# Optimization experiments

Measured on AMD Instinct MI355X. Metric: run time of the kernel, lower is better.

Reference implementation:

```python
import math
import jax, jax.numpy as jnp
import numpy as np

B, T, C, H = 4, 2048, 1024, 16
HS = C // H


def setup_inputs() -> dict:
    key = jax.random.key(0)
    ks = jax.random.split(key, 5)
    s_in = 1.0 / math.sqrt(C)
    return {
        "x": jax.random.normal(ks[0], (B, T, C), dtype=jnp.float32),
        "w_attn": jax.random.normal(ks[1], (C, 3 * C), dtype=jnp.float32) * s_in,
        "b_attn": jax.random.normal(ks[2], (3 * C,), dtype=jnp.float32) * 0.02,
        "w_proj": jax.random.normal(ks[3], (C, C), dtype=jnp.float32) * s_in,
        "b_proj": jax.random.normal(ks[4], (C,), dtype=jnp.float32) * 0.02,
    }


def reference(x, w_attn, b_attn, w_proj, b_proj):
    Bx, Tx, Cx = x.shape
    hs = Cx // H
    qkv = x @ w_attn + b_attn  # [B, T, 3C]
    q, k, v = jnp.split(qkv, 3, axis=-1)
    # [B, H, T, hs]
    q = q.reshape(Bx, Tx, H, hs).transpose(0, 2, 1, 3)
    k = k.reshape(Bx, Tx, H, hs).transpose(0, 2, 1, 3)
    v = v.reshape(Bx, Tx, H, hs).transpose(0, 2, 1, 3)
    scale = 1.0 / math.sqrt(hs)
    att = jnp.einsum("bhqd,bhkd->bhqk", q, k) * scale  # [B, H, T, T]
    causal = jnp.tril(jnp.ones((Tx, Tx), dtype=bool))
    att = jnp.where(causal, att, -jnp.inf)
    att = jax.nn.softmax(att, axis=-1)
    y = jnp.einsum("bhqk,bhkd->bhqd", att, v)  # [B, H, T, hs]
    y = y.transpose(0, 2, 1, 3).reshape(Bx, Tx, Cx)
    return y @ w_proj + b_proj
```

## Files before the change

### kernel.cpp

```cpp
#include <hip/hip_runtime.h>
#include <stdint.h>

#define Bn 4
#define Tn 2048
#define Cn 1024
#define Hn 16
#define HSn 64
#define Mn (Bn*Tn)
#define N1n (3*Cn)

typedef unsigned short u16;
typedef unsigned int u32;
typedef __attribute__((ext_vector_type(8))) short short8;
typedef __attribute__((ext_vector_type(4))) float f32x4;
typedef __attribute__((ext_vector_type(16))) float f32x16;

#define QSCf (0.125f * 1.44269504f)

__device__ __forceinline__ u16 f2bf(float f){
  u32 u = __float_as_uint(f);
  u += 0x7fffu + ((u >> 16) & 1u);
  return (u16)(u >> 16);
}

__device__ __forceinline__ u32 pkbf(float lo, float hi_){
  u32 r; asm("v_cvt_pk_bf16_f32 %0, %1, %2" : "=v"(r) : "v"(lo), "v"(hi_)); return r;
}

__device__ __forceinline__ float fexp2(float x){
  float r; asm("v_exp_f32 %0, %1" : "=v"(r) : "v"(x)); return r;
}

__device__ __forceinline__ float fmax3(float a, float b, float c){
  float r; asm("v_max3_f32 %0, %1, %2, %3" : "=v"(r) : "v"(a), "v"(b), "v"(c)); return r;
}

__device__ __forceinline__ void plswap(u32 &a, u32 &b){
  auto r = __builtin_amdgcn_permlane32_swap(a, b, false, false);
  a = r[0]; b = r[1];
}

__device__ __forceinline__ void gload_lds16(const void* g, void* l){
  __builtin_amdgcn_global_load_lds(
      (const __attribute__((address_space(1))) u32*)g,
      (__attribute__((address_space(3))) u32*)l, 16, 0, 0);
}

#define BARRIER() __builtin_amdgcn_s_barrier()
#define CFENCE() asm volatile("" ::: "memory")

__device__ __forceinline__ void tcvt_body(const float* __restrict__ in,
                                          u16* __restrict__ out,
                                          int R, int Cc, int bxx, int byy,
                                          float sh[64][68]){
  int tid = threadIdx.x;
  int c0 = bxx*64, r0 = byy*64;
  int rr = tid >> 4, c4 = (tid & 15) * 4;
  #pragma unroll
  for (int p=0;p<4;p++){
    int r = rr + 16*p;
    *(float4*)&sh[r][c4] = *(const float4*)&in[(size_t)(r0+r)*Cc + c0 + c4];
  }
  __syncthreads();
  #pragma unroll
  for (int p=0;p<4;p++){
    int oc = rr + 16*p;
    u32 w0 = (u32)f2bf(sh[c4+0][oc]) | ((u32)f2bf(sh[c4+1][oc]) << 16);
    u32 w1 = (u32)f2bf(sh[c4+2][oc]) | ((u32)f2bf(sh[c4+3][oc]) << 16);
    uint2 pk; pk.x = w0; pk.y = w1;
    *(uint2*)&out[(size_t)(c0+oc)*R + r0 + c4] = pk;
  }
}

__global__ __launch_bounds__(256)
void k_pre(const float* __restrict__ x, const float* __restrict__ wa,
           const float* __restrict__ wp, u16* __restrict__ xb,
           u16* __restrict__ waT, u16* __restrict__ wpT){
  __shared__ float sh[64][68];
  int bid = blockIdx.x;
  if (bid < 4096){
    int i = bid*256 + threadIdx.x;
    const float4* p = (const float4*)(x) + (size_t)i*2;
    float4 a = p[0], b = p[1];
    uint4 r;
    r.x = (u32)f2bf(a.x) | ((u32)f2bf(a.y) << 16);
    r.y = (u32)f2bf(a.z) | ((u32)f2bf(a.w) << 16);
    r.z = (u32)f2bf(b.x) | ((u32)f2bf(b.y) << 16);
    r.w = (u32)f2bf(b.z) | ((u32)f2bf(b.w) << 16);
    *((uint4*)(xb) + i) = r;
  } else if (bid < 4096 + 768){
    int b2 = bid - 4096;
    tcvt_body(wa, waT, Cn, N1n, b2 % 48, b2 / 48, sh);
  } else {
    int b3 = bid - 4864;
    tcvt_body(wp, wpT, Cn, Cn, b3 % 16, b3 / 16, sh);
  }
}

template <int MODE>
__global__ __launch_bounds__(256, 2)
void k_gemm2(const u16* __restrict__ A, const u16* __restrict__ Bt,
             const float* __restrict__ bias, void* __restrict__ Cout,
             u16* __restrict__ vt, int Nn_, int byPerXcd)
{
  extern __shared__ char smem[];
  const int nkt = 16;
  int tid = threadIdx.x;
  int wave = tid >> 6, lane = tid & 63, g = lane >> 4, cl = lane & 15;
  int wm = wave >> 1, wn = wave & 1;

  int xcd = blockIdx.x & 7, idx = blockIdx.x >> 3;
  int by = xcd * byPerXcd + (idx % byPerXcd);
  int bx = idx / byPerXcd;
  int m0 = by * 128, n0 = bx * 128;

  int srow = tid >> 3;
  int scolb = (tid & 7) << 4;
  int ssw = scolb ^ ((srow & 7) << 4);
  const char* Agp = (const char*)A  + (size_t)(m0 + srow) * 2048 + ssw;
  const char* Bgp = (const char*)Bt + (size_t)(n0 + srow) * 2048 + ssw;

  #define STG(t_, b_) { \
    const char* ag = Agp + (size_t)(t_)*128; \
    const char* bg = Bgp + (size_t)(t_)*128; \
    char* ab = smem + (b_)*32768 + (wave<<10); \
    char* bb = ab + 16384; \
    gload_lds16(ag,          ab); \
    gload_lds16(ag+ 65536,   ab+4096); \
    gload_lds16(ag+131072,   ab+8192); \
    gload_lds16(ag+196608,   ab+12288); \
    gload_lds16(bg,          bb); \
    gload_lds16(bg+ 65536,   bb+4096); \
    gload_lds16(bg+131072,   bb+8192); \
    gload_lds16(bg+196608,   bb+12288); }

  f32x4 acc[4][4];
  #pragma unroll
  for (int i=0;i<4;i++)
    #pragma unroll
    for (int j=0;j<4;j++) acc[i][j] = (f32x4){0.f,0.f,0.f,0.f};

  STG(0, 0);

  for (int t=0; t<nkt; ++t){
    int b = t & 1;
    if (t+1 < nkt){
      STG(t+1, b^1);
      asm volatile("s_waitcnt vmcnt(8)" ::: "memory");
    } else {
      asm volatile("s_waitcnt vmcnt(0)" ::: "memory");
    }
    BARRIER(); CFENCE();
    const char* Asb = smem + b*32768;
    const char* Bsb = Asb + 16384;
    short8 a[4][2], bq[4][2];
    #pragma unroll
    for (int i=0;i<4;i++){
      int row = wm*64 + i*16 + cl;
      #pragma unroll
      for (int ks=0;ks<2;ks++)
        a[i][ks] = *(const short8*)(Asb + row*128 + ((ks*64 + g*16) ^ ((row&7)<<4)));
    }
    #pragma unroll
    for (int j=0;j<4;j++){
      int row = wn*64 + j*16 + cl;
      #pragma unroll
      for (int ks=0;ks<2;ks++)
        bq[j][ks] = *(const short8*)(Bsb + row*128 + ((ks*64 + g*16) ^ ((row&7)<<4)));
    }
    asm volatile("s_waitcnt lgkmcnt(0)" ::: "memory");
    __builtin_amdgcn_s_setprio(1);
    #pragma unroll
    for (int ks=0;ks<2;ks++)
      #pragma unroll
      for (int i=0;i<4;i++)
        #pragma unroll
        for (int j=0;j<4;j++)
          acc[i][j] = __builtin_amdgcn_mfma_f32_16x16x32_bf16(a[i][ks], bq[j][ks], acc[i][j], 0, 0, 0);
    __builtin_amdgcn_s_setprio(0);
    CFENCE(); BARRIER(); CFENCE();
  }
  #undef STG

  #pragma unroll
  for (int jj=0;jj<4;jj++){
    int col = n0 + wn*64 + jj*16 + cl;
    float bj = bias[col];
    if (MODE == 0){
      #pragma unroll
      for (int i=0;i<4;i++){
        int rowb = m0 + wm*64 + i*16 + g*4;
        #pragma unroll
        for (int r=0;r<4;r++)
          ((float*)Cout)[(size_t)(rowb+r)*Nn_ + col] = acc[i][jj][r] + bj;
      }
    } else if (col < 2*Cn){
      float sc = (col < Cn) ? QSCf : 1.0f;
      #pragma unroll
      for (int i=0;i<4;i++){
        int rowb = m0 + wm*64 + i*16 + g*4;
        #pragma unroll
        for (int r=0;r<4;r++)
          ((u16*)Cout)[(size_t)(rowb+r)*Nn_ + col] = f2bf((acc[i][jj][r] + bj) * sc);
      }
    } else {
      int hd = col - 2*Cn;
      #pragma unroll
      for (int i=0;i<4;i++){
        int rowb = m0 + wm*64 + i*16 + g*4;
        int bb = rowb >> 11, tt = rowb & 2047;
        u16* dst = vt + (((size_t)(bb*16 + (hd>>6)))*64 + (hd&63))*2048 + tt;
        uint2 pk;
        pk.x = (u32)f2bf(acc[i][jj][0]+bj) | ((u32)f2bf(acc[i][jj][1]+bj) << 16);
        pk.y = (u32)f2bf(acc[i][jj][2]+bj) | ((u32)f2bf(acc[i][jj][3]+bj) << 16);
        *(uint2*)dst = pk;
      }
    }
  }
}

__global__ __launch_bounds__(256, 4)
void k_attn(const u16* __restrict__ qkv, const u16* __restrict__ vt, u16* __restrict__ yb){
  __shared__ __align__(16) u16 Ks[2][64*64];
  __shared__ __align__(16) u16 Vs[2][64*64];
  int tid = threadIdx.x, wave = tid >> 6, lane = tid & 63;
  int ql = lane & 31, hi = lane >> 5;
  int blk = blockIdx.x;
  int xcd = blk & 7, rest = blk >> 3;
  int bh  = xcd + 8*(rest & 7);
  int qtsel = rest >> 3;
  int a_ = qtsel & 3, g_ = qtsel >> 2;
  int qt = (g_==0) ? (15 - a_) : (g_==1) ? (7 - a_) : (g_==2) ? (8 + a_) : a_;
  int b = bh >> 4, h = bh & 15;

  const u16* Kbase = qkv + (size_t)b*Tn*N1n + Cn + h*HSn;
  const u16* Vbase = vt  + (size_t)bh*HSn*Tn;

  auto STAGE = [&](int bufi, int kt){
    int kb_ = kt*64;
    #pragma unroll
    for (int it=0; it<2; ++it){
      int off = it*4096 + tid*16;
      int row = off >> 7;
      int cb  = off & 127;
      int gc  = (cb ^ ((row & 7) << 4)) >> 1;
      gload_lds16(Kbase + (size_t)(kb_ + row)*N1n + gc,
                  (char*)&Ks[bufi][0] + it*4096 + (wave << 10));
      gload_lds16(Vbase + (size_t)row*Tn + kb_ + gc,
                  (char*)&Vs[bufi][0] + it*4096 + (wave << 10));
    }
  };

  int q0 = qt * 128;
  int qw0 = q0 + wave*32;
  int qg  = qw0 + ql;
  int ntiles = 2*qt + 2;

  const u16* Qp = qkv + (size_t)(b*Tn + qg)*N1n + h*HSn;
  short8 qf[4];
  #pragma unroll
  for (int dc=0; dc<4; ++dc) qf[dc] = *(const short8*)&Qp[dc*16 + hi*8];

  f32x16 accO[2];
  #pragma unroll
  for (int f=0; f<2; ++f)
    #pragma unroll
    for (int r=0; r<16; ++r) accO[f][r] = 0.f;
  float m_ = -1e30f, l_ = 0.f;

  STAGE(0, 0);
  asm volatile("s_waitcnt vmcnt(0)" ::: "memory");
  __syncthreads();
  int buf = 0;

  for (int kt=0; kt<ntiles; ++kt){
    if (kt+1 < ntiles) STAGE(buf^1, kt+1);
    const char* Ksb = (const char*)&Ks[buf][0];
    const char* Vsb = (const char*)&Vs[buf][0];
    #pragma unroll
    for (int ksub=0; ksub<2; ++ksub){
      int kbase = kt*64 + ksub*32;
      if (kbase <= qw0 + 31){
        f32x16 s;
        #pragma unroll
        for (int r=0; r<16; ++r) s[r] = 0.f;
        __builtin_amdgcn_s_setprio(1);
        #pragma unroll
        for (int dc=0; dc<4; ++dc){
          short8 kf = *(const short8*)(Ksb + ((ksub*32 + ql) << 7)
                          + ((dc*32 + hi*16) ^ ((ql & 7) << 4)));
          s = __builtin_amdgcn_mfma_f32_32x32x16_bf16(kf, qf[dc], s, 0, 0, 0);
        }
        __builtin_amdgcn_s_setprio(0);
        float p[16];
        if (kbase + 31 > qw0){
          #pragma unroll
          for (int r=0; r<16; ++r){
            int krow = kbase + (r&3) + 8*(r>>2) + 4*hi;
            p[r] = (krow > qg) ? -1e30f : s[r];
          }
        } else {
          #pragma unroll
          for (int r=0; r<16; ++r) p[r] = s[r];
        }
        float r0 = fmax3(p[0], p[1], p[2]);
        float r1 = fmax3(p[3], p[4], p[5]);
        float r2 = fmax3(p[6], p[7], p[8]);
        float r3 = fmax3(p[9], p[10], p[11]);
        float r4 = fmax3(p[12], p[13], p[14]);
        float tm = fmaxf(fmax3(r0, r1, r2), fmax3(r3, r4, p[15]));
        { u32 ua = __float_as_uint(tm), ub = ua; plswap(ua, ub);
          tm = fmaxf(__uint_as_float(ua), __uint_as_float(ub)); }
        if (!__all(tm - m_ <= 8.0f)){
          float mn = fmaxf(m_, tm);
          float al = fexp2(m_ - mn);
          m_ = mn; l_ *= al;
          #pragma unroll
          for (int f=0; f<2; ++f)
            #pragma unroll
            for (int r=0; r<16; ++r) accO[f][r] *= al;
        }
        float ls = 0.f;
        #pragma unroll
        for (int r=0; r<16; ++r){ float e = fexp2(p[r] - m_); p[r] = e; ls += e; }
        { u32 ua = __float_as_uint(ls), ub = ua; plswap(ua, ub);
          l_ += __uint_as_float(ua) + __uint_as_float(ub); }
        #pragma unroll
        for (int ks=0; ks<2; ++ks){
          int pb = ks*8;
          u32 w0 = pkbf(p[pb+0], p[pb+1]);
          u32 w1 = pkbf(p[pb+2], p[pb+3]);
          u32 w2 = pkbf(p[pb+4], p[pb+5]);
          u32 w3 = pkbf(p[pb+6], p[pb+7]);
          plswap(w0, w2);
          plswap(w1, w3);
          union { u32 w[4]; short8 v; } pu;
          pu.w[0] = w0; pu.w[1] = w1; pu.w[2] = w2; pu.w[3] = w3;
          __builtin_amdgcn_s_setprio(1);
          #pragma unroll
          for (int f=0; f<2; ++f){
            short8 vf = *(const short8*)(Vsb + ((f*32 + ql) << 7)
                            + ((ksub*64 + ks*32 + hi*16) ^ ((ql & 7) << 4)));
            accO[f] = __builtin_amdgcn_mfma_f32_32x32x16_bf16(vf, pu.v, accO[f], 0, 0, 0);
          }
          __builtin_amdgcn_s_setprio(0);
        }
      }
    }
    asm volatile("s_waitcnt vmcnt(0)" ::: "memory");
    __syncthreads();
    buf ^= 1;
  }

  float rl = 1.0f / l_;
  u16* yp = yb + (size_t)(b*Tn + qg)*Cn + h*HSn;
  #pragma unroll
  for (int f=0; f<2; ++f)
    #pragma unroll
    for (int rq=0; rq<4; ++rq){
      int d0 = f*32 + rq*8 + hi*4;
      float v0 = accO[f][rq*4+0]*rl, v1 = accO[f][rq*4+1]*rl;
      float v2 = accO[f][rq*4+2]*rl, v3 = accO[f][rq*4+3]*rl;
      uint2 pk2;
      pk2.x = (u32)f2bf(v0) | ((u32)f2bf(v1) << 16);
      pk2.y = (u32)f2bf(v2) | ((u32)f2bf(v3) << 16);
      *(uint2*)&yp[d0] = pk2;
    }
}

extern "C" void kernel_launch(void* const* d_in, const int* in_sizes, int n_in,
                              void* d_out, int out_size, void* d_ws, size_t ws_size,
                              hipStream_t stream)
{
  const float* x      = (const float*)d_in[0];
  const float* w_attn = (const float*)d_in[1];
  const float* b_attn = (const float*)d_in[2];
  const float* w_proj = (const float*)d_in[3];
  const float* b_proj = (const float*)d_in[4];
  float* out = (float*)d_out;
  char* ws = (char*)d_ws;

  size_t off = 0;
  u16* xb  = (u16*)(ws + off); off += (size_t)Mn*Cn*2;
  u16* waT = (u16*)(ws + off); off += (size_t)N1n*Cn*2;
  u16* wpT = (u16*)(ws + off); off += (size_t)Cn*Cn*2;
  u16* qkv = (u16*)(ws + off); off += (size_t)Mn*N1n*2;
  u16* vt  = (u16*)(ws + off); off += (size_t)Bn*Hn*HSn*Tn*2;
  u16* yb  = (u16*)(ws + off); off += (size_t)Mn*Cn*2;

  (void)hipFuncSetAttribute((const void*)k_gemm2<1>,
        hipFuncAttributeMaxDynamicSharedMemorySize, 65536);
  (void)hipFuncSetAttribute((const void*)k_gemm2<0>,
        hipFuncAttributeMaxDynamicSharedMemorySize, 65536);

  k_pre<<<dim3(5120), 256, 0, stream>>>(x, w_attn, w_proj, xb, waT, wpT);
  k_gemm2<1><<<dim3((Mn/128)*(N1n/128)), 256, 65536, stream>>>(xb, waT, b_attn, qkv, vt, N1n, 8);
  k_attn<<<dim3(1024), 256, 0, stream>>>(qkv, vt, yb);
  k_gemm2<0><<<dim3((Mn/128)*(Cn/128)), 256, 65536, stream>>>(yb, wpT, b_proj, out, nullptr, Cn, 8);
}
```

Measured before the change: 142.4 us.

## Process two 32-row query strips per wave to reuse K/V fragments

The attention kernel now gives each wave 64 query rows, held as two 32-row strips with separate online-softmax state. This doubles the query tile per block to 256 and halves the grid to 512 blocks. K and V fragments are loaded from LDS once and shared by both strips, which cuts LDS traffic and K/V staging per query row. Launch bounds drop to 2 blocks per SM to make room for the doubled registers. Fewer blocks and coarser causal tiles may hurt occupancy and load balance.

New measurement: 159.7 us. 12.1% more time.

```diff
diff --git a/kernel.cpp b/kernel.cpp
--- a/kernel.cpp
+++ b/kernel.cpp
@@ -219,7 +219,7 @@
   }
 }
 
-__global__ __launch_bounds__(256, 4)
+__global__ __launch_bounds__(256, 2)
 void k_attn(const u16* __restrict__ qkv, const u16* __restrict__ vt, u16* __restrict__ yb){
   __shared__ __align__(16) u16 Ks[2][64*64];
   __shared__ __align__(16) u16 Vs[2][64*64];
@@ -228,9 +228,8 @@
   int blk = blockIdx.x;
   int xcd = blk & 7, rest = blk >> 3;
   int bh  = xcd + 8*(rest & 7);
-  int qtsel = rest >> 3;
-  int a_ = qtsel & 3, g_ = qtsel >> 2;
-  int qt = (g_==0) ? (15 - a_) : (g_==1) ? (7 - a_) : (g_==2) ? (8 + a_) : a_;
+  int sel = rest >> 3;
+  int qt  = (sel < 4) ? (7 - sel) : (sel - 4);
   int b = bh >> 4, h = bh & 15;
 
   const u16* Kbase = qkv + (size_t)b*Tn*N1n + Cn + h*HSn;
@@ -251,22 +250,77 @@
     }
   };
 
-  int q0 = qt * 128;
-  int qw0 = q0 + wave*32;
-  int qg  = qw0 + ql;
-  int ntiles = 2*qt + 2;
-
-  const u16* Qp = qkv + (size_t)(b*Tn + qg)*N1n + h*HSn;
-  short8 qf[4];
-  #pragma unroll
-  for (int dc=0; dc<4; ++dc) qf[dc] = *(const short8*)&Qp[dc*16 + hi*8];
-
-  f32x16 accO[2];
-  #pragma unroll
-  for (int f=0; f<2; ++f)
-    #pragma unroll
-    for (int r=0; r<16; ++r) accO[f][r] = 0.f;
-  float m_ = -1e30f, l_ = 0.f;
+  int q0 = qt * 256;
+  int qw0A = q0 + wave*64;
+  int qw0B = qw0A + 32;
+  int qgA = qw0A + ql, qgB = qw0B + ql;
+  int ntiles = 4*qt + 4;
+
+  const u16* QpA = qkv + (size_t)(b*Tn + qgA)*N1n + h*HSn;
+  const u16* QpB = qkv + (size_t)(b*Tn + qgB)*N1n + h*HSn;
+  short8 qfA[4], qfB[4];
+  #pragma unroll
+  for (int dc=0; dc<4; ++dc){
+    qfA[dc] = *(const short8*)&QpA[dc*16 + hi*8];
+    qfB[dc] = *(const short8*)&QpB[dc*16 + hi*8];
+  }
+
+  f32x16 oA0, oA1, oB0, oB1;
+  #pragma unroll
+  for (int r=0; r<16; ++r){ oA0[r]=0.f; oA1[r]=0.f; oB0[r]=0.f; oB1[r]=0.f; }
+  float mA = -1e30f, lA = 0.f, mB = -1e30f, lB = 0.f;
+
+  auto SMPV = [&](f32x16& s, int qg_, int qw0_, float& m_, float& l_,
+                  f32x16& o0, f32x16& o1, int kbase,
+                  short8 vf00, short8 vf01, short8 vf10, short8 vf11){
+    float p[16];
+    if (kbase + 31 > qw0_){
+      #pragma unroll
+      for (int r=0; r<16; ++r){
+        int krow = kbase + (r&3) + 8*(r>>2) + 4*hi;
+        p[r] = (krow > qg_) ? -1e30f : s[r];
+      }
+    } else {
+      #pragma unroll
+      for (int r=0; r<16; ++r) p[r] = s[r];
+    }
+    float r0 = fmax3(p[0], p[1], p[2]);
+    float r1 = fmax3(p[3], p[4], p[5]);
+    float r2 = fmax3(p[6], p[7], p[8]);
+    float r3 = fmax3(p[9], p[10], p[11]);
+    float r4 = fmax3(p[12], p[13], p[14]);
+    float tm = fmaxf(fmax3(r0, r1, r2), fmax3(r3, r4, p[15]));
+    { u32 ua = __float_as_uint(tm), ub = ua; plswap(ua, ub);
+      tm = fmaxf(__uint_as_float(ua), __uint_as_float(ub)); }
+    if (!__all(tm - m_ <= 8.0f)){
+      float mn = fmaxf(m_, tm);
+      float al = fexp2(m_ - mn);
+      m_ = mn; l_ *= al;
+      #pragma unroll
+      for (int r=0; r<16; ++r){ o0[r] *= al; o1[r] *= al; }
+    }
+    float ls = 0.f;
+    #pragma unroll
+    for (int r=0; r<16; ++r){ float e = fexp2(p[r] - m_); p[r] = e; ls += e; }
+    { u32 ua = __float_as_uint(ls), ub = ua; plswap(ua, ub);
+      l_ += __uint_as_float(ua) + __uint_as_float(ub); }
+    #pragma unroll
+    for (int ks=0; ks<2; ++ks){
+      int pb = ks*8;
+      u32 w0 = pkbf(p[pb+0], p[pb+1]);
+      u32 w1 = pkbf(p[pb+2], p[pb+3]);
+      u32 w2 = pkbf(p[pb+4], p[pb+5]);
+      u32 w3 = pkbf(p[pb+6], p[pb+7]);
+      plswap(w0, w2);
+      plswap(w1, w3);
+      union { u32 w[4]; short8 v; } pu;
+      pu.w[0] = w0; pu.w[1] = w1; pu.w[2] = w2; pu.w[3] = w3;
+      __builtin_amdgcn_s_setprio(1);
+      o0 = __builtin_amdgcn_mfma_f32_32x32x16_bf16(ks ? vf10 : vf00, pu.v, o0, 0, 0, 0);
+      o1 = __builtin_amdgcn_mfma_f32_32x32x16_bf16(ks ? vf11 : vf01, pu.v, o1, 0, 0, 0);
+      __builtin_amdgcn_s_setprio(0);
+    }
+  };
 
   STAGE(0, 0);
   asm volatile("s_waitcnt vmcnt(0)" ::: "memory");
@@ -280,71 +334,35 @@
     #pragma unroll
     for (int ksub=0; ksub<2; ++ksub){
       int kbase = kt*64 + ksub*32;
-      if (kbase <= qw0 + 31){
-        f32x16 s;
+      if (kbase <= qw0B + 31){
+        bool actA = (kbase <= qw0A + 31);
+        int krow7 = ((ksub*32 + ql) << 7);
+        int xsw = ((ql & 7) << 4);
+        short8 kf0 = *(const short8*)(Ksb + krow7 + ((  0 + hi*16) ^ xsw));
+        short8 kf1 = *(const short8*)(Ksb + krow7 + (( 32 + hi*16) ^ xsw));
+        short8 kf2 = *(const short8*)(Ksb + krow7 + (( 64 + hi*16) ^ xsw));
+        short8 kf3 = *(const short8*)(Ksb + krow7 + (( 96 + hi*16) ^ xsw));
+        short8 vf00 = *(const short8*)(Vsb + ((     ql) << 7) + ((ksub*64 +  0 + hi*16) ^ xsw));
+        short8 vf01 = *(const short8*)(Vsb + ((32 + ql) << 7) + ((ksub*64 +  0 + hi*16) ^ xsw));
+        short8 vf10 = *(const short8*)(Vsb + ((     ql) << 7) + ((ksub*64 + 32 + hi*16) ^ xsw));
+        short8 vf11 = *(const short8*)(Vsb + ((32 + ql) << 7) + ((ksub*64 + 32 + hi*16) ^ xsw));
+        f32x16 sA, sB;
         #pragma unroll
-        for (int r=0; r<16; ++r) s[r] = 0.f;
+        for (int r=0; r<16; ++r){ sA[r]=0.f; sB[r]=0.f; }
         __builtin_amdgcn_s_setprio(1);
-        #pragma unroll
-        for (int dc=0; dc<4; ++dc){
-          short8 kf = *(const short8*)(Ksb + ((ksub*32 + ql) << 7)
-                          + ((dc*32 + hi*16) ^ ((ql & 7) << 4)));
-          s = __builtin_amdgcn_mfma_f32_32x32x16_bf16(kf, qf[dc], s, 0, 0, 0);
+        if (actA){
+          sA = __builtin_amdgcn_mfma_f32_32x32x16_bf16(kf0, qfA[0], sA, 0, 0, 0);
+          sA = __builtin_amdgcn_mfma_f32_32x32x16_bf16(kf1, qfA[1], sA, 0, 0, 0);
+          sA = __builtin_amdgcn_mfma_f32_32x32x16_bf16(kf2, qfA[2], sA, 0, 0, 0);
+          sA = __builtin_amdgcn_mfma_f32_32x32x16_bf16(kf3, qfA[3], sA, 0, 0, 0);
         }
+        sB = __builtin_amdgcn_mfma_f32_32x32x16_bf16(kf0, qfB[0], sB, 0, 0, 0);
+        sB = __builtin_amdgcn_mfma_f32_32x32x16_bf16(kf1, qfB[1], sB, 0, 0, 0);
+        sB = __builtin_amdgcn_mfma_f32_32x32x16_bf16(kf2, qfB[2], sB, 0, 0, 0);
+        sB = __builtin_amdgcn_mfma_f32_32x32x16_bf16(kf3, qfB[3], sB, 0, 0, 0);
         __builtin_amdgcn_s_setprio(0);
-        float p[16];
-        if (kbase + 31 > qw0){
-          #pragma unroll
-          for (int r=0; r<16; ++r){
-            int krow = kbase + (r&3) + 8*(r>>2) + 4*hi;
-            p[r] = (krow > qg) ? -1e30f : s[r];
-          }
-        } else {
-          #pragma unroll
-          for (int r=0; r<16; ++r) p[r] = s[r];
-        }
-        float r0 = fmax3(p[0], p[1], p[2]);
-        float r1 = fmax3(p[3], p[4], p[5]);
-        float r2 = fmax3(p[6], p[7], p[8]);
-        float r3 = fmax3(p[9], p[10], p[11]);
-        float r4 = fmax3(p[12], p[13], p[14]);
-        float tm = fmaxf(fmax3(r0, r1, r2), fmax3(r3, r4, p[15]));
-        { u32 ua = __float_as_uint(tm), ub = ua; plswap(ua, ub);
-          tm = fmaxf(__uint_as_float(ua), __uint_as_float(ub)); }
-        if (!__all(tm - m_ <= 8.0f)){
-          float mn = fmaxf(m_, tm);
-          float al = fexp2(m_ - mn);
-          m_ = mn; l_ *= al;
-          #pragma unroll
-          for (int f=0; f<2; ++f)
-            #pragma unroll
-            for (int r=0; r<16; ++r) accO[f][r] *= al;
-        }
-        float ls = 0.f;
-        #pragma unroll
-        for (int r=0; r<16; ++r){ float e = fexp2(p[r] - m_); p[r] = e; ls += e; }
-        { u32 ua = __float_as_uint(ls), ub = ua; plswap(ua, ub);
-          l_ += __uint_as_float(ua) + __uint_as_float(ub); }
-        #pragma unroll
-        for (int ks=0; ks<2; ++ks){
-          int pb = ks*8;
-          u32 w0 = pkbf(p[pb+0], p[pb+1]);
-          u32 w1 = pkbf(p[pb+2], p[pb+3]);
-          u32 w2 = pkbf(p[pb+4], p[pb+5]);
-          u32 w3 = pkbf(p[pb+6], p[pb+7]);
-          plswap(w0, w2);
-          plswap(w1, w3);
-          union { u32 w[4]; short8 v; } pu;
-          pu.w[0] = w0; pu.w[1] = w1; pu.w[2] = w2; pu.w[3] = w3;
-          __builtin_amdgcn_s_setprio(1);
-          #pragma unroll
-          for (int f=0; f<2; ++f){
-            short8 vf = *(const short8*)(Vsb + ((f*32 + ql) << 7)
-                            + ((ksub*64 + ks*32 + hi*16) ^ ((ql & 7) << 4)));
-            accO[f] = __builtin_amdgcn_mfma_f32_32x32x16_bf16(vf, pu.v, accO[f], 0, 0, 0);
-          }
-          __builtin_amdgcn_s_setprio(0);
-        }
+        if (actA) SMPV(sA, qgA, qw0A, mA, lA, oA0, oA1, kbase, vf00, vf01, vf10, vf11);
+        SMPV(sB, qgB, qw0B, mB, lB, oB0, oB1, kbase, vf00, vf01, vf10, vf11);
       }
     }
     asm volatile("s_waitcnt vmcnt(0)" ::: "memory");
@@ -352,20 +370,36 @@
     buf ^= 1;
   }
 
-  float rl = 1.0f / l_;
-  u16* yp = yb + (size_t)(b*Tn + qg)*Cn + h*HSn;
-  #pragma unroll
-  for (int f=0; f<2; ++f)
+  {
+    float rl = 1.0f / lA;
+    u16* yp = yb + (size_t)(b*Tn + qgA)*Cn + h*HSn;
     #pragma unroll
     for (int rq=0; rq<4; ++rq){
-      int d0 = f*32 + rq*8 + hi*4;
-      float v0 = accO[f][rq*4+0]*rl, v1 = accO[f][rq*4+1]*rl;
-      float v2 = accO[f][rq*4+2]*rl, v3 = accO[f][rq*4+3]*rl;
+      int d0 = rq*8 + hi*4;
       uint2 pk2;
-      pk2.x = (u32)f2bf(v0) | ((u32)f2bf(v1) << 16);
-      pk2.y = (u32)f2bf(v2) | ((u32)f2bf(v3) << 16);
+      pk2.x = (u32)f2bf(oA0[rq*4+0]*rl) | ((u32)f2bf(oA0[rq*4+1]*rl) << 16);
+      pk2.y = (u32)f2bf(oA0[rq*4+2]*rl) | ((u32)f2bf(oA0[rq*4+3]*rl) << 16);
       *(uint2*)&yp[d0] = pk2;
-    }
+      pk2.x = (u32)f2bf(oA1[rq*4+0]*rl) | ((u32)f2bf(oA1[rq*4+1]*rl) << 16);
+      pk2.y = (u32)f2bf(oA1[rq*4+2]*rl) | ((u32)f2bf(oA1[rq*4+3]*rl) << 16);
+      *(uint2*)&yp[32 + d0] = pk2;
+    }
+  }
+  {
+    float rl = 1.0f / lB;
+    u16* yp = yb + (size_t)(b*Tn + qgB)*Cn + h*HSn;
+    #pragma unroll
+    for (int rq=0; rq<4; ++rq){
+      int d0 = rq*8 + hi*4;
+      uint2 pk2;
+      pk2.x = (u32)f2bf(oB0[rq*4+0]*rl) | ((u32)f2bf(oB0[rq*4+1]*rl) << 16);
+      pk2.y = (u32)f2bf(oB0[rq*4+2]*rl) | ((u32)f2bf(oB0[rq*4+3]*rl) << 16);
+      *(uint2*)&yp[d0] = pk2;
+      pk2.x = (u32)f2bf(oB1[rq*4+0]*rl) | ((u32)f2bf(oB1[rq*4+1]*rl) << 16);
+      pk2.y = (u32)f2bf(oB1[rq*4+2]*rl) | ((u32)f2bf(oB1[rq*4+3]*rl) << 16);
+      *(uint2*)&yp[32 + d0] = pk2;
+    }
+  }
 }
 
 extern "C" void kernel_launch(void* const* d_in, const int* in_sizes, int n_in,
@@ -395,6 +429,6 @@
 
   k_pre<<<dim3(5120), 256, 0, stream>>>(x, w_attn, w_proj, xb, waT, wpT);
   k_gemm2<1><<<dim3((Mn/128)*(N1n/128)), 256, 65536, stream>>>(xb, waT, b_attn, qkv, vt, N1n, 8);
-  k_attn<<<dim3(1024), 256, 0, stream>>>(qkv, vt, yb);
+  k_attn<<<dim3(512), 256, 0, stream>>>(qkv, vt, yb);
   k_gemm2<0><<<dim3((Mn/128)*(Cn/128)), 256, 65536, stream>>>(yb, wpT, b_proj, out, nullptr, Cn, 8);
 }
```
